# Kernel tuning notes

Measured on AMD Instinct MI355X. Metric: run time of the kernel, lower is better.

Reference implementation:

```python
import jax, jax.numpy as jnp
import numpy as np

NUM_EXPERTS = 8
TOP_K = 2
HIDDEN = 2048
FFN = 4096


def setup_inputs() -> dict:
    key = jax.random.key(0)
    ks = jax.random.split(key, 5)
    s = 0.02
    return {
        "hidden_states": jax.random.normal(ks[0], (2, 2048, HIDDEN), dtype=jnp.float32),
        "w_router": jax.random.normal(ks[1], (HIDDEN, NUM_EXPERTS), dtype=jnp.float32) * s,
        "w1": jax.random.normal(ks[2], (NUM_EXPERTS, FFN, HIDDEN), dtype=jnp.float32) * s,
        "w2": jax.random.normal(ks[3], (NUM_EXPERTS, HIDDEN, FFN), dtype=jnp.float32) * s,
        "w3": jax.random.normal(ks[4], (NUM_EXPERTS, FFN, HIDDEN), dtype=jnp.float32) * s,
    }


def reference(hidden_states, w_router, w1, w2, w3):
    shape = hidden_states.shape
    x = hidden_states.reshape(-1, HIDDEN)  # [T, H]

    # Router: logits -> softmax -> top-k -> renormalize (Mixtral routing)
    logits = x @ w_router                              # [T, E]
    probs = jax.nn.softmax(logits, axis=-1)
    top_w, top_i = jax.lax.top_k(probs, TOP_K)         # [T, K]
    top_w = top_w / jnp.sum(top_w, axis=-1, keepdims=True)
    # Dense combine weights per expert: [T, E]
    combine = jnp.sum(
        jax.nn.one_hot(top_i, NUM_EXPERTS, dtype=x.dtype) * top_w[..., None], axis=1
    )

    # Grouped SwiGLU experts: out = sum_e combine[:, e] * w2_e(silu(w1_e x) * w3_e x)
    out = jnp.zeros_like(x)
    for e in range(NUM_EXPERTS):
        h = jax.nn.silu(x @ w1[e].T) * (x @ w3[e].T)   # [T, F]
        y = h @ w2[e].T                                # [T, H]
        out = out + combine[:, e:e + 1] * y

    return (out.reshape(shape), jnp.zeros((1,), dtype=x.dtype))
```

## Files before the change

kernel.cpp:

```cpp
#include <hip/hip_runtime.h>
#include <hip/hip_bf16.h>
#include <stdint.h>

#define T_TOK 4096
#define HID   2048
#define FFN_D 4096
#define NE    8
#define PADB  256

typedef __attribute__((ext_vector_type(8))) short  short8;
typedef __attribute__((ext_vector_type(4))) float  f32x4;
typedef __attribute__((ext_vector_type(4))) unsigned short u16x4;
typedef unsigned short u16;

__device__ __forceinline__ u16 f2bf(float f) {
    unsigned u = __float_as_uint(f);
    u += 0x7FFFu + ((u >> 16) & 1u);
    return (u16)(u >> 16);
}
__device__ __forceinline__ float bf2f(u16 v) {
    return __uint_as_float(((unsigned)v) << 16);
}

__device__ __forceinline__ short8 cvt8(f32x4 a, f32x4 b) {
    union { unsigned u[4]; short8 s; } r;
    asm("v_cvt_pk_bf16_f32 %0, %1, %2" : "=v"(r.u[0]) : "v"(a[0]), "v"(a[1]));
    asm("v_cvt_pk_bf16_f32 %0, %1, %2" : "=v"(r.u[1]) : "v"(a[2]), "v"(a[3]));
    asm("v_cvt_pk_bf16_f32 %0, %1, %2" : "=v"(r.u[2]) : "v"(b[0]), "v"(b[1]));
    asm("v_cvt_pk_bf16_f32 %0, %1, %2" : "=v"(r.u[3]) : "v"(b[2]), "v"(b[3]));
    return r.s;
}

#define GLD16(g, l) __builtin_amdgcn_global_load_lds( \
    (const __attribute__((address_space(1))) unsigned int*)(g), \
    (__attribute__((address_space(3))) unsigned int*)(l), 16, 0, 0)

__global__ void k_convert(const float* __restrict__ s, u16* __restrict__ d, long n8) {
    for (long i = (long)blockIdx.x * 256 + threadIdx.x; i < n8; i += (long)gridDim.x * 256) {
        f32x4 a = *((const f32x4*)s + i * 2);
        f32x4 b = *((const f32x4*)s + i * 2 + 1);
        short8 o;
#pragma unroll
        for (int q = 0; q < 4; ++q) { o[q] = (short)f2bf(a[q]); o[q + 4] = (short)f2bf(b[q]); }
        *(short8*)(d + i * 8) = o;
    }
}

__global__ void k_router(const float* __restrict__ x, const float* __restrict__ wr,
                         int* __restrict__ topk_id, float* __restrict__ topk_w,
                         int* __restrict__ counts) {
    int lane = threadIdx.x & 63;
    int t = blockIdx.x * 4 + (threadIdx.x >> 6);
    const float* xr = x + (size_t)t * HID;
    float acc[8];
#pragma unroll
    for (int e = 0; e < 8; ++e) acc[e] = 0.f;
    for (int h = lane; h < HID; h += 64) {
        float xv = xr[h];
        f32x4 w0 = *(const f32x4*)(wr + h * 8);
        f32x4 w1 = *(const f32x4*)(wr + h * 8 + 4);
#pragma unroll
        for (int q = 0; q < 4; ++q) { acc[q] += xv * w0[q]; acc[4 + q] += xv * w1[q]; }
    }
#pragma unroll
    for (int e = 0; e < 8; ++e) {
        float v = acc[e];
#pragma unroll
        for (int s = 32; s > 0; s >>= 1) v += __shfl_xor(v, s);
        acc[e] = v;
    }
    if (lane == 0) {
        int i0 = 0; float l0 = acc[0];
#pragma unroll
        for (int e = 1; e < 8; ++e) if (acc[e] > l0) { l0 = acc[e]; i0 = e; }
        int i1 = -1; float l1 = -3.4e38f;
#pragma unroll
        for (int e = 0; e < 8; ++e) if (e != i0 && acc[e] > l1) { l1 = acc[e]; i1 = e; }
        float wA = 1.f / (1.f + expf(l1 - l0));
        topk_id[t * 2] = i0;  topk_id[t * 2 + 1] = i1;
        topk_w[t * 2] = wA;   topk_w[t * 2 + 1] = 1.f - wA;
        atomicAdd(&counts[i0], 1);
        atomicAdd(&counts[i1], 1);
    }
}

__global__ void k_scan(const int* __restrict__ counts, int* __restrict__ pad_off,
                       int* __restrict__ perm_tok) {
    __shared__ int sTot;
    if (threadIdx.x == 0) {
        int o = 0;
#pragma unroll
        for (int e = 0; e < 8; ++e) { pad_off[e] = o; o += ((counts[e] + PADB - 1) / PADB) * PADB; }
        pad_off[8] = o; sTot = o;
    }
    __syncthreads();
    int tot = sTot;
    for (int i = threadIdx.x; i < tot; i += 256) perm_tok[i] = 0;
}

__global__ void k_scatter(const int* __restrict__ topk_id, int* __restrict__ cursors,
                          const int* __restrict__ pad_off, int* __restrict__ perm_tok,
                          int* __restrict__ pos_of) {
    int t = blockIdx.x * 256 + threadIdx.x;
    if (t >= T_TOK) return;
#pragma unroll
    for (int k = 0; k < 2; ++k) {
        int e = topk_id[t * 2 + k];
        int p = pad_off[e] + atomicAdd(&cursors[e], 1);
        perm_tok[p] = t;
        pos_of[t * 2 + k] = p;
    }
}

template<int KTOT, int NTOT, bool DUAL, bool GATHER>
__global__ __launch_bounds__(512, 2) void k_gemm8f(
    const u16* __restrict__ A,
    const float* __restrict__ B0all,
    const float* __restrict__ B1all,
    u16* __restrict__ C,
    const int* __restrict__ perm_tok,
    const int* __restrict__ pad_off)
{
    constexpr int BMt   = 256;
    constexpr int BNt   = DUAL ? 128 : 256;
    constexpr int NI    = DUAL ? 2 : 4;
    constexpr int WCW   = DUAL ? 32 : 64;
    constexpr int CPX   = (NTOT / BNt) / 8;
    constexpr int NK    = KTOT / 64;
    constexpr int ATILE = BMt * 64;
    constexpr int BTILE = BNt * 64;

    const int bid = blockIdx.x;
    const int xcd = bid & 7;
    const int idx = bid >> 3;
    const int m0  = (idx / CPX) * BMt;
    if (m0 >= pad_off[8]) return;
    const int n0  = (xcd * CPX + (idx % CPX)) * BNt;
    int e = 0;
    while (pad_off[e + 1] <= m0) ++e;

    __shared__ u16 As[2 * ATILE];
    __shared__ u16 Bs0[2 * BTILE];
    __shared__ u16 Bs1[DUAL ? 2 * BTILE : 8];
    __shared__ int tokS[GATHER ? BMt : 8];

    const int tid = threadIdx.x;
    const int w = tid >> 6, l = tid & 63;
    if (GATHER) {
        for (int i = tid; i < BMt; i += 512) tokS[i] = perm_tok[m0 + i];
        __syncthreads();
    }

    const float* B0 = B0all + (size_t)e * NTOT * KTOT;
    const float* B1 = DUAL ? (B1all + (size_t)e * NTOT * KTOT) : B0all;

    const int lr = l >> 3;
    const int c  = (l & 7) ^ lr;

    const u16* aSrc[4];
    u16* aDst[4];
#pragma unroll
    for (int ja = 0; ja < 4; ++ja) {
        const int row = w * 32 + ja * 8 + lr;
        const long ar = GATHER ? (long)tokS[row] : (long)(m0 + row);
        aSrc[ja] = A + ar * KTOT + c * 8;
        aDst[ja] = (u16*)As + (w * 32 + ja * 8) * 64;
    }

    const float* Bg = DUAL ? (w < 4 ? B0 : B1) : B0;
    u16* bL = DUAL ? (w < 4 ? (u16*)Bs0 : (u16*)Bs1) : (u16*)Bs0;
    const int bBase = DUAL ? (w & 3) * 32 : w * 32;
    const float* bSrc[4];
    u16* bDst[4];
#pragma unroll
    for (int jb = 0; jb < 4; ++jb) {
        const int rowb = bBase + jb * 8 + lr;
        bSrc[jb] = Bg + (size_t)(n0 + rowb) * KTOT + c * 8;
        bDst[jb] = bL + (bBase + jb * 8) * 64 + l * 8;
    }

    const int wr = w >> 2, wc = w & 3;
    const int fr = l & 15, fk = l >> 4, x7 = l & 7;
    const int pc0 = ((fk ^ x7) << 3);
    const int pc1 = pc0 ^ 32;
    const int aB = (wr * 128 + fr) * 64;
    const int bB = (wc * WCW + fr) * 64;

    f32x4 acc0[8][NI], acc1[8][NI];
    const f32x4 fz = {0.f, 0.f, 0.f, 0.f};
#pragma unroll
    for (int mi = 0; mi < 8; ++mi)
#pragma unroll
        for (int ni = 0; ni < NI; ++ni) { acc0[mi][ni] = fz; if (DUAL) acc1[mi][ni] = fz; }

    f32x4 br[8];

#pragma unroll
    for (int jb = 0; jb < 4; ++jb) {
        br[2 * jb]     = ((const f32x4*)bSrc[jb])[0];
        br[2 * jb + 1] = ((const f32x4*)bSrc[jb])[1];
    }
#pragma unroll
    for (int ja = 0; ja < 4; ++ja) GLD16(aSrc[ja], aDst[ja]);
#pragma unroll
    for (int jb = 0; jb < 4; ++jb)
        *(short8*)(bDst[jb]) = cvt8(br[2 * jb], br[2 * jb + 1]);
    asm volatile("s_waitcnt vmcnt(0) lgkmcnt(0)" ::: "memory");
    __builtin_amdgcn_s_barrier();
    __builtin_amdgcn_sched_barrier(0);

#pragma unroll 1
    for (int t = 0; t < NK; ++t) {
        const int cb = t & 1, nb = cb ^ 1;
        const long kE = (long)(t + 1) * 64;
        const bool hasNext = (t + 1 < NK);
        const u16* aC  = (const u16*)As  + cb * ATILE;
        const u16* b0C = (const u16*)Bs0 + cb * BTILE;
        const u16* b1C = (const u16*)Bs1 + (DUAL ? cb * BTILE : 0);

        if (hasNext) {
#pragma unroll
            for (int jb = 0; jb < 4; ++jb) {
                const f32x4* p = (const f32x4*)(bSrc[jb] + kE);
                br[2 * jb]     = p[0];
                br[2 * jb + 1] = p[1];
            }
#pragma unroll
            for (int ja = 0; ja < 4; ++ja) GLD16(aSrc[ja] + kE, aDst[ja] + nb * ATILE);
        }
        __builtin_amdgcn_sched_barrier(0);

        short8 af[4], b0f[NI], b1f[NI];

#pragma unroll
        for (int mi = 0; mi < 4; ++mi) af[mi] = *(const short8*)(aC + aB + mi * 1024 + pc0);
#pragma unroll
        for (int ni = 0; ni < NI; ++ni) {
            b0f[ni] = *(const short8*)(b0C + bB + ni * 1024 + pc0);
            if (DUAL) b1f[ni] = *(const short8*)(b1C + bB + ni * 1024 + pc0);
        }
        __builtin_amdgcn_s_setprio(1);
#pragma unroll
        for (int mi = 0; mi < 4; ++mi)
#pragma unroll
            for (int ni = 0; ni < NI; ++ni) {
                acc0[mi][ni] = __builtin_amdgcn_mfma_f32_16x16x32_bf16(af[mi], b0f[ni], acc0[mi][ni], 0, 0, 0);
                if (DUAL)
                    acc1[mi][ni] = __builtin_amdgcn_mfma_f32_16x16x32_bf16(af[mi], b1f[ni], acc1[mi][ni], 0, 0, 0);
            }
        __builtin_amdgcn_s_setprio(0);

#pragma unroll
        for (int mi = 0; mi < 4; ++mi) af[mi] = *(const short8*)(aC + aB + (mi + 4) * 1024 + pc0);
        __builtin_amdgcn_s_setprio(1);
#pragma unroll
        for (int mi = 0; mi < 4; ++mi)
#pragma unroll
            for (int ni = 0; ni < NI; ++ni) {
                acc0[mi + 4][ni] = __builtin_amdgcn_mfma_f32_16x16x32_bf16(af[mi], b0f[ni], acc0[mi + 4][ni], 0, 0, 0);
                if (DUAL)
                    acc1[mi + 4][ni] = __builtin_amdgcn_mfma_f32_16x16x32_bf16(af[mi], b1f[ni], acc1[mi + 4][ni], 0, 0, 0);
            }
        __builtin_amdgcn_s_setprio(0);

#pragma unroll
        for (int mi = 0; mi < 4; ++mi) af[mi] = *(const short8*)(aC + aB + mi * 1024 + pc1);
#pragma unroll
        for (int ni = 0; ni < NI; ++ni) {
            b0f[ni] = *(const short8*)(b0C + bB + ni * 1024 + pc1);
            if (DUAL) b1f[ni] = *(const short8*)(b1C + bB + ni * 1024 + pc1);
        }
        __builtin_amdgcn_s_setprio(1);
#pragma unroll
        for (int mi = 0; mi < 4; ++mi)
#pragma unroll
            for (int ni = 0; ni < NI; ++ni) {
                acc0[mi][ni] = __builtin_amdgcn_mfma_f32_16x16x32_bf16(af[mi], b0f[ni], acc0[mi][ni], 0, 0, 0);
                if (DUAL)
                    acc1[mi][ni] = __builtin_amdgcn_mfma_f32_16x16x32_bf16(af[mi], b1f[ni], acc1[mi][ni], 0, 0, 0);
            }
        __builtin_amdgcn_s_setprio(0);

#pragma unroll
        for (int mi = 0; mi < 4; ++mi) af[mi] = *(const short8*)(aC + aB + (mi + 4) * 1024 + pc1);
        __builtin_amdgcn_s_setprio(1);
#pragma unroll
        for (int mi = 0; mi < 4; ++mi)
#pragma unroll
            for (int ni = 0; ni < NI; ++ni) {
                acc0[mi + 4][ni] = __builtin_amdgcn_mfma_f32_16x16x32_bf16(af[mi], b0f[ni], acc0[mi + 4][ni], 0, 0, 0);
                if (DUAL)
                    acc1[mi + 4][ni] = __builtin_amdgcn_mfma_f32_16x16x32_bf16(af[mi], b1f[ni], acc1[mi + 4][ni], 0, 0, 0);
            }
        __builtin_amdgcn_s_setprio(0);
        __builtin_amdgcn_sched_barrier(0);

        if (hasNext) {
#pragma unroll
            for (int jb = 0; jb < 4; ++jb)
                *(short8*)(bDst[jb] + nb * BTILE) = cvt8(br[2 * jb], br[2 * jb + 1]);
        }

        asm volatile("s_waitcnt vmcnt(0) lgkmcnt(0)" ::: "memory");
        __builtin_amdgcn_s_barrier();
        __builtin_amdgcn_sched_barrier(0);
    }

    const int er = (l >> 4) * 4;
    const int ec = l & 15;
#pragma unroll
    for (int mi = 0; mi < 8; ++mi)
#pragma unroll
        for (int ni = 0; ni < NI; ++ni)
#pragma unroll
            for (int r = 0; r < 4; ++r) {
                size_t prow = (size_t)(m0 + wr * 128 + mi * 16 + er + r);
                int col = n0 + wc * WCW + ni * 16 + ec;
                float v = acc0[mi][ni][r];
                float res;
                if (DUAL) {
                    float g3 = acc1[mi][ni][r];
                    res = v / (1.f + __expf(-v)) * g3;
                } else {
                    res = v;
                }
                C[prow * NTOT + col] = f2bf(res);
            }
}

__global__ void k_combine(const u16* __restrict__ y, const int* __restrict__ pos_of,
                          const float* __restrict__ topk_w, float* __restrict__ out) {
    int idx = blockIdx.x * 256 + threadIdx.x;
    int t  = idx >> 9;
    int c4 = (idx & 511) << 2;
    int p0 = pos_of[t * 2], p1 = pos_of[t * 2 + 1];
    float w0 = topk_w[t * 2], w1 = topk_w[t * 2 + 1];
    u16x4 a = *(const u16x4*)(y + (size_t)p0 * HID + c4);
    u16x4 b = *(const u16x4*)(y + (size_t)p1 * HID + c4);
    f32x4 o;
#pragma unroll
    for (int q = 0; q < 4; ++q) o[q] = w0 * bf2f(a[q]) + w1 * bf2f(b[q]);
    *(f32x4*)(out + (size_t)t * HID + c4) = o;
    if (idx == 0) out[(size_t)T_TOK * HID] = 0.f;
}

__global__ void k_init(int* __restrict__ c) {
    if (threadIdx.x < 16) c[threadIdx.x] = 0;
}

extern "C" void kernel_launch(void* const* d_in, const int* in_sizes, int n_in,
                              void* d_out, int out_size, void* d_ws, size_t ws_size,
                              hipStream_t stream) {
    const float* x  = (const float*)d_in[0];
    const float* wr = (const float*)d_in[1];
    const float* w1 = (const float*)d_in[2];
    const float* w2 = (const float*)d_in[3];
    const float* w3 = (const float*)d_in[4];
    float* out = (float*)d_out;
    char* ws = (char*)d_ws;

    u16*  xb  = (u16*)(ws);
    u16*  hb  = (u16*)(ws + 16777216);
    u16*  yb  = (u16*)(ws + 100663296);
    int*  perm_tok = (int*)(ws + 142606336);
    int*  pos_of   = (int*)(ws + 142647296);
    int*  topk_id  = (int*)(ws + 142680064);
    float* topk_w  = (float*)(ws + 142712832);
    int*  cnt      = (int*)(ws + 142745600);
    int*  counts   = cnt;
    int*  cursors  = cnt + 8;
    int*  pad_off  = cnt + 16;

    k_init<<<1, 64, 0, stream>>>(cnt);
    k_convert<<<2048, 256, 0, stream>>>(x, xb, (long)T_TOK * HID / 8);
    k_router<<<1024, 256, 0, stream>>>(x, wr, topk_id, topk_w, counts);
    k_scan<<<1, 256, 0, stream>>>(counts, pad_off, perm_tok);
    k_scatter<<<16, 256, 0, stream>>>(topk_id, cursors, pad_off, perm_tok, pos_of);

    k_gemm8f<HID, FFN_D, true, true><<<(FFN_D / 128) * 40, 512, 0, stream>>>(
        xb, w1, w3, hb, perm_tok, pad_off);

    k_gemm8f<FFN_D, HID, false, false><<<(HID / 256) * 40, 512, 0, stream>>>(
        hb, w2, (const float*)nullptr, yb, perm_tok, pad_off);

    k_combine<<<8192, 256, 0, stream>>>(yb, pos_of, topk_w, out);
}
```

Baseline: 1.010 ms.

## Preconvert expert weights to bf16 and load both GEMM operands via direct-to-LDS

Adds separate passes converting w1, w3 and w2 to bf16 in workspace before the expert GEMMs. The GEMM kernel then loads both A and B tiles with global_load_lds, removing the in-loop fp32 register loads and conversions. It also splits the issue of those loads across the first and second MFMA halves. The down-projection GEMM now uses 128-wide N tiles. This adds extra full-weight conversion traffic and a larger workspace in exchange for halving the weight bytes each GEMM block fetches.

```diff
diff --git a/kernel.cpp b/kernel.cpp
--- a/kernel.cpp
+++ b/kernel.cpp
@@ -20,15 +20,6 @@
 }
 __device__ __forceinline__ float bf2f(u16 v) {
     return __uint_as_float(((unsigned)v) << 16);
-}
-
-__device__ __forceinline__ short8 cvt8(f32x4 a, f32x4 b) {
-    union { unsigned u[4]; short8 s; } r;
-    asm("v_cvt_pk_bf16_f32 %0, %1, %2" : "=v"(r.u[0]) : "v"(a[0]), "v"(a[1]));
-    asm("v_cvt_pk_bf16_f32 %0, %1, %2" : "=v"(r.u[1]) : "v"(a[2]), "v"(a[3]));
-    asm("v_cvt_pk_bf16_f32 %0, %1, %2" : "=v"(r.u[2]) : "v"(b[0]), "v"(b[1]));
-    asm("v_cvt_pk_bf16_f32 %0, %1, %2" : "=v"(r.u[3]) : "v"(b[2]), "v"(b[3]));
-    return r.s;
 }
 
 #define GLD16(g, l) __builtin_amdgcn_global_load_lds( \
@@ -112,23 +103,23 @@
     }
 }
 
-template<int KTOT, int NTOT, bool DUAL, bool GATHER>
-__global__ __launch_bounds__(512, 2) void k_gemm8f(
+template<int KTOT, int NTOT, int BNt, bool DUAL, bool GATHER>
+__global__ __launch_bounds__(512, 2) void k_gemm8(
     const u16* __restrict__ A,
-    const float* __restrict__ B0all,
-    const float* __restrict__ B1all,
+    const u16* __restrict__ B0all,
+    const u16* __restrict__ B1all,
     u16* __restrict__ C,
     const int* __restrict__ perm_tok,
     const int* __restrict__ pad_off)
 {
     constexpr int BMt   = 256;
-    constexpr int BNt   = DUAL ? 128 : 256;
-    constexpr int NI    = DUAL ? 2 : 4;
-    constexpr int WCW   = DUAL ? 32 : 64;
+    constexpr int WCW   = BNt / 4;
+    constexpr int NI    = WCW / 16;
     constexpr int CPX   = (NTOT / BNt) / 8;
     constexpr int NK    = KTOT / 64;
     constexpr int ATILE = BMt * 64;
     constexpr int BTILE = BNt * 64;
+    constexpr int SEGB  = DUAL ? 8 : (BNt == 256 ? 8 : 4);
 
     const int bid = blockIdx.x;
     const int xcd = bid & 7;
@@ -151,32 +142,39 @@
         __syncthreads();
     }
 
-    const float* B0 = B0all + (size_t)e * NTOT * KTOT;
-    const float* B1 = DUAL ? (B1all + (size_t)e * NTOT * KTOT) : B0all;
-
-    const int lr = l >> 3;
-    const int c  = (l & 7) ^ lr;
-
-    const u16* aSrc[4];
-    u16* aDst[4];
-#pragma unroll
-    for (int ja = 0; ja < 4; ++ja) {
-        const int row = w * 32 + ja * 8 + lr;
-        const long ar = GATHER ? (long)tokS[row] : (long)(m0 + row);
-        aSrc[ja] = A + ar * KTOT + c * 8;
-        aDst[ja] = (u16*)As + (w * 32 + ja * 8) * 64;
-    }
-
-    const float* Bg = DUAL ? (w < 4 ? B0 : B1) : B0;
-    u16* bL = DUAL ? (w < 4 ? (u16*)Bs0 : (u16*)Bs1) : (u16*)Bs0;
-    const int bBase = DUAL ? (w & 3) * 32 : w * 32;
-    const float* bSrc[4];
-    u16* bDst[4];
-#pragma unroll
-    for (int jb = 0; jb < 4; ++jb) {
-        const int rowb = bBase + jb * 8 + lr;
-        bSrc[jb] = Bg + (size_t)(n0 + rowb) * KTOT + c * 8;
-        bDst[jb] = bL + (bBase + jb * 8) * 64 + l * 8;
+    const u16* B0 = B0all + (size_t)e * NTOT * KTOT;
+    const u16* B1 = DUAL ? (B1all + (size_t)e * NTOT * KTOT) : B0all;
+
+    const int nseg = (w < 4) ? 8 : SEGB;
+    const u16* gsrc[8];
+    u16* ldst[8];
+    int tstep;
+    {
+        const int c = (l & 7) ^ (l >> 3);
+#pragma unroll
+        for (int j = 0; j < 8; ++j) {
+            const int js = (j < nseg) ? j : (j - 4);
+            const int rl = js * 8 + (l >> 3);
+            if (w < 4) {
+                const int rt = w * 64 + rl;
+                const long grow = GATHER ? (long)tokS[rt] : (long)(m0 + rt);
+                gsrc[j] = A + grow * KTOT + c * 8;
+                ldst[j] = (u16*)As + (w * 64 + js * 8) * 64;
+                tstep = ATILE;
+            } else if (DUAL && w >= 6) {
+                const int rt = (w - 6) * 64 + rl;
+                gsrc[j] = B1 + (size_t)(n0 + rt) * KTOT + c * 8;
+                ldst[j] = (u16*)Bs1 + (rt - rl + js * 8) * 64;
+                tstep = BTILE;
+            } else {
+                const int rt = DUAL ? ((w - 4) * 64 + rl)
+                                    : (BNt == 256 ? ((w - 4) * 64 + rl)
+                                                  : ((w - 4) * 32 + rl));
+                gsrc[j] = B0 + (size_t)(n0 + rt) * KTOT + c * 8;
+                ldst[j] = (u16*)Bs0 + (rt - rl + js * 8) * 64;
+                tstep = BTILE;
+            }
+        }
     }
 
     const int wr = w >> 2, wc = w & 3;
@@ -193,45 +191,27 @@
 #pragma unroll
         for (int ni = 0; ni < NI; ++ni) { acc0[mi][ni] = fz; if (DUAL) acc1[mi][ni] = fz; }
 
-    f32x4 br[8];
-
-#pragma unroll
-    for (int jb = 0; jb < 4; ++jb) {
-        br[2 * jb]     = ((const f32x4*)bSrc[jb])[0];
-        br[2 * jb + 1] = ((const f32x4*)bSrc[jb])[1];
-    }
-#pragma unroll
-    for (int ja = 0; ja < 4; ++ja) GLD16(aSrc[ja], aDst[ja]);
-#pragma unroll
-    for (int jb = 0; jb < 4; ++jb)
-        *(short8*)(bDst[jb]) = cvt8(br[2 * jb], br[2 * jb + 1]);
-    asm volatile("s_waitcnt vmcnt(0) lgkmcnt(0)" ::: "memory");
+#pragma unroll
+    for (int j = 0; j < 8; ++j) if (j < nseg) GLD16(gsrc[j], ldst[j]);
+    asm volatile("s_waitcnt vmcnt(0)" ::: "memory");
     __builtin_amdgcn_s_barrier();
     __builtin_amdgcn_sched_barrier(0);
 
 #pragma unroll 1
     for (int t = 0; t < NK; ++t) {
-        const int cb = t & 1, nb = cb ^ 1;
-        const long kE = (long)(t + 1) * 64;
-        const bool hasNext = (t + 1 < NK);
+        const int cb = t & 1, nb2 = cb ^ 1;
         const u16* aC  = (const u16*)As  + cb * ATILE;
         const u16* b0C = (const u16*)Bs0 + cb * BTILE;
         const u16* b1C = (const u16*)Bs1 + (DUAL ? cb * BTILE : 0);
+        const long kE = (long)(t + 1) * 64;
+        const bool hasNext = (t + 1 < NK);
+
+        short8 af[4], b0f[NI], b1f[NI];
 
         if (hasNext) {
 #pragma unroll
-            for (int jb = 0; jb < 4; ++jb) {
-                const f32x4* p = (const f32x4*)(bSrc[jb] + kE);
-                br[2 * jb]     = p[0];
-                br[2 * jb + 1] = p[1];
-            }
-#pragma unroll
-            for (int ja = 0; ja < 4; ++ja) GLD16(aSrc[ja] + kE, aDst[ja] + nb * ATILE);
-        }
-        __builtin_amdgcn_sched_barrier(0);
-
-        short8 af[4], b0f[NI], b1f[NI];
-
+            for (int j = 0; j < 4; ++j) if (j < nseg) GLD16(gsrc[j] + kE, ldst[j] + nb2 * tstep);
+        }
 #pragma unroll
         for (int mi = 0; mi < 4; ++mi) af[mi] = *(const short8*)(aC + aB + mi * 1024 + pc0);
 #pragma unroll
@@ -250,6 +230,10 @@
             }
         __builtin_amdgcn_s_setprio(0);
 
+        if (hasNext) {
+#pragma unroll
+            for (int j = 4; j < 8; ++j) if (j < nseg) GLD16(gsrc[j] + kE, ldst[j] + nb2 * tstep);
+        }
 #pragma unroll
         for (int mi = 0; mi < 4; ++mi) af[mi] = *(const short8*)(aC + aB + (mi + 4) * 1024 + pc0);
         __builtin_amdgcn_s_setprio(1);
@@ -293,15 +277,8 @@
                     acc1[mi + 4][ni] = __builtin_amdgcn_mfma_f32_16x16x32_bf16(af[mi], b1f[ni], acc1[mi + 4][ni], 0, 0, 0);
             }
         __builtin_amdgcn_s_setprio(0);
-        __builtin_amdgcn_sched_barrier(0);
-
-        if (hasNext) {
-#pragma unroll
-            for (int jb = 0; jb < 4; ++jb)
-                *(short8*)(bDst[jb] + nb * BTILE) = cvt8(br[2 * jb], br[2 * jb + 1]);
-        }
-
-        asm volatile("s_waitcnt vmcnt(0) lgkmcnt(0)" ::: "memory");
+
+        asm volatile("s_waitcnt vmcnt(0)" ::: "memory");
         __builtin_amdgcn_s_barrier();
         __builtin_amdgcn_sched_barrier(0);
     }
@@ -360,13 +337,15 @@
     char* ws = (char*)d_ws;
 
     u16*  xb  = (u16*)(ws);
-    u16*  hb  = (u16*)(ws + 16777216);
-    u16*  yb  = (u16*)(ws + 100663296);
-    int*  perm_tok = (int*)(ws + 142606336);
-    int*  pos_of   = (int*)(ws + 142647296);
-    int*  topk_id  = (int*)(ws + 142680064);
-    float* topk_w  = (float*)(ws + 142712832);
-    int*  cnt      = (int*)(ws + 142745600);
+    u16*  wA  = (u16*)(ws + 16777216);
+    u16*  w3b = (u16*)(ws + 150994944);
+    u16*  hb  = (u16*)(ws + 285212672);
+    u16*  yb  = (u16*)(ws + 150994944);
+    int*  perm_tok = (int*)(ws + 369098752);
+    int*  pos_of   = (int*)(ws + 369139712);
+    int*  topk_id  = (int*)(ws + 369172480);
+    float* topk_w  = (float*)(ws + 369205248);
+    int*  cnt      = (int*)(ws + 369238016);
     int*  counts   = cnt;
     int*  cursors  = cnt + 8;
     int*  pad_off  = cnt + 16;
@@ -377,11 +356,17 @@
     k_scan<<<1, 256, 0, stream>>>(counts, pad_off, perm_tok);
     k_scatter<<<16, 256, 0, stream>>>(topk_id, cursors, pad_off, perm_tok, pos_of);
 
-    k_gemm8f<HID, FFN_D, true, true><<<(FFN_D / 128) * 40, 512, 0, stream>>>(
-        xb, w1, w3, hb, perm_tok, pad_off);
-
-    k_gemm8f<FFN_D, HID, false, false><<<(HID / 256) * 40, 512, 0, stream>>>(
-        hb, w2, (const float*)nullptr, yb, perm_tok, pad_off);
+    const long WN8 = (long)NE * FFN_D * HID / 8;
+    k_convert<<<4096, 256, 0, stream>>>(w1, wA, WN8);
+    k_convert<<<4096, 256, 0, stream>>>(w3, w3b, WN8);
+
+    k_gemm8<HID, FFN_D, 128, true, true><<<(FFN_D / 128) * 40, 512, 0, stream>>>(
+        xb, wA, w3b, hb, perm_tok, pad_off);
+
+    k_convert<<<4096, 256, 0, stream>>>(w2, wA, WN8);
+
+    k_gemm8<FFN_D, HID, 128, false, false><<<(HID / 128) * 40, 512, 0, stream>>>(
+        hb, wA, (const u16*)nullptr, yb, perm_tok, pad_off);
 
     k_combine<<<8192, 256, 0, stream>>>(yb, pos_of, topk_w, out);
 }
```

Result: faster. 946.5 us (-6.3%).
